# Performance work log

Hardware: AMD Instinct MI355X
Metric: run time of the kernel (lower is better)

Reference implementation:

```python
import jax, jax.numpy as jnp
import numpy as np

B, T, A, S = 8, 64, 4, 512
V, EXT_V = 32000, 33000  # base vocab, base + OOV extensions


def setup_inputs() -> dict:
    key = jax.random.key(0)
    k1, k2, k3, k4, k5 = jax.random.split(key, 5)
    vocab_probs = jax.random.uniform(k1, (B, T, V), dtype=jnp.float32)
    vocab_probs = vocab_probs / vocab_probs.sum(-1, keepdims=True)
    generation_probs = jax.random.uniform(k2, (B, T, A), dtype=jnp.float32)
    agentwise_attn = jax.random.uniform(k3, (B, T, A, S), dtype=jnp.float32)
    agentwise_attn = agentwise_attn / agentwise_attn.sum(-1, keepdims=True)
    agent_attn = jax.random.uniform(k4, (B, T, A), dtype=jnp.float32)
    agent_attn = agent_attn / agent_attn.sum(-1, keepdims=True)
    article = jax.random.randint(k5, (B, A, S), 0, EXT_V, dtype=jnp.int64)
    return {
        "vocab_probs": vocab_probs,
        "generation_probs": generation_probs,
        "agentwise_attn": agentwise_attn,
        "agent_attn": agent_attn,
        "article": article,
    }


def reference(vocab_probs, generation_probs, agentwise_attn, agent_attn, article):
    # vocab_probs: [B,T,V], generation_probs/agent_attn: [B,T,A],
    # agentwise_attn: [B,T,A,S], article: [B,A,S] int indices < EXT_V
    gen = generation_probs[..., None]                       # [B,T,A,1]
    voc_gen = gen * vocab_probs[:, :, None, :]              # [B,T,A,V]
    copy = (1.0 - gen) * agentwise_attn                     # [B,T,A,S]
    # concat-with-zeros pad to extended vocab
    ext = jnp.concatenate(
        [voc_gen, jnp.zeros((B, T, A, EXT_V - V), voc_gen.dtype)], axis=-1
    )                                                       # [B,T,A,EXT_V]
    # scatter_add copy probs at article token positions (expanded over tgt_len)
    idx = jnp.broadcast_to(article[:, None, :, :], (B, T, A, S))
    bi = jnp.arange(B)[:, None, None, None]
    ti = jnp.arange(T)[None, :, None, None]
    ai = jnp.arange(A)[None, None, :, None]
    ext = ext.at[bi, ti, ai, idx].add(copy)
    # agent-attention weighted sum over agents
    return jnp.einsum("bta,btav->btv", agent_attn, ext)     # [B,T,EXT_V]
```

## Files before the change

### kernel.cpp

```cpp
#include <hip/hip_runtime.h>
#include <hip/hip_bf16.h>

constexpr int B = 8, T = 64, A = 4, S = 512;
constexpr int V = 32000, EXT_V = 33000;
constexpr int V4 = V / 4;
constexpr int HALF = EXT_V / 2;
constexpr int H4 = HALF / 4;
constexpr int NTHREADS = 1024;

__global__ void __launch_bounds__(NTHREADS, 2)
fused_kernel(const float* __restrict__ vocab,
             const float* __restrict__ gen,
             const float* __restrict__ attn,
             const float* __restrict__ agent_attn,
             const int* __restrict__ article,
             float* __restrict__ out) {
    __shared__ float smem[HALF];
    const int blk = blockIdx.x;
    const int bt = blk >> 1;
    const int half = blk & 1;
    const int vbase = half * HALF;
    const int b = bt / T;
    const int tid = threadIdx.x;

    float4* s4 = reinterpret_cast<float4*>(smem);
    for (int i = tid; i < H4; i += NTHREADS)
        s4[i] = make_float4(0.f, 0.f, 0.f, 0.f);

    float coef = 0.f;
#pragma unroll
    for (int a = 0; a < A; ++a)
        coef += agent_attn[bt * A + a] * gen[bt * A + a];

    __syncthreads();

#pragma unroll
    for (int k = 0; k < (A * S) / NTHREADS; ++k) {
        const int j = tid + k * NTHREADS;
        const int a = j >> 9;
        const int s = j & (S - 1);
        const int bta = bt * A + a;
        const int idx = article[(b * A + a) * S + s] - vbase;
        if ((unsigned)idx < (unsigned)HALF) {
            const float g = gen[bta];
            const float w = agent_attn[bta] * (1.0f - g);
            const float val = w * attn[(size_t)bta * S + s];
            atomicAdd(smem + idx, val);
        }
    }
    __syncthreads();

    const float4* __restrict__ vrow = reinterpret_cast<const float4*>(vocab + (size_t)bt * V);
    float4* __restrict__ orow = reinterpret_cast<float4*>(out + (size_t)bt * EXT_V);
    const int g4base = vbase / 4;
    for (int i = tid; i < H4; i += NTHREADS) {
        const int gi = g4base + i;
        float4 r = s4[i];
        if (gi < V4) {
            const float4 x = vrow[gi];
            r.x += x.x * coef;
            r.y += x.y * coef;
            r.z += x.z * coef;
            r.w += x.w * coef;
        }
        orow[gi] = r;
    }
}

extern "C" void kernel_launch(void* const* d_in, const int* in_sizes, int n_in,
                              void* d_out, int out_size, void* d_ws, size_t ws_size,
                              hipStream_t stream) {
    const float* vocab      = (const float*)d_in[0];
    const float* gen        = (const float*)d_in[1];
    const float* attn       = (const float*)d_in[2];
    const float* agent_attn = (const float*)d_in[3];
    const int*   article    = (const int*)d_in[4];
    float* out = (float*)d_out;

    fused_kernel<<<2 * B * T, NTHREADS, 0, stream>>>(vocab, gen, attn, agent_attn, article, out);
}
```

Before: 124.6 us.

## Prefetch scatter inputs and first vocab tiles before smem zeroing; remap blocks per XCD

Loads the article indices, attention values and agent weights for the scatter, plus the first two float4 vocab chunks per thread, into registers before the shared-memory clear and first barrier. This hides global-load latency behind the zeroing and the atomics. It also remaps blockIdx so consecutive logical blocks land on the same XCD, which should improve L2 locality for the shared article/gen data. The cost is more live registers under a 1024-thread, 2-blocks-per-CU launch bound.

```diff
diff --git a/kernel.cpp b/kernel.cpp
--- a/kernel.cpp
+++ b/kernel.cpp
@@ -7,6 +7,7 @@
 constexpr int HALF = EXT_V / 2;
 constexpr int H4 = HALF / 4;
 constexpr int NTHREADS = 1024;
+constexpr int NBLK = 2 * B * T;
 
 __global__ void __launch_bounds__(NTHREADS, 2)
 fused_kernel(const float* __restrict__ vocab,
@@ -16,52 +17,65 @@
              const int* __restrict__ article,
              float* __restrict__ out) {
     __shared__ float smem[HALF];
-    const int blk = blockIdx.x;
-    const int bt = blk >> 1;
-    const int half = blk & 1;
+    constexpr int PER_XCD = NBLK / 8;
+    const int l = (blockIdx.x & 7) * PER_XCD + (blockIdx.x >> 3);
+    const int bt = l >> 1;
+    const int half = l & 1;
     const int vbase = half * HALF;
     const int b = bt / T;
     const int tid = threadIdx.x;
 
-    float4* s4 = reinterpret_cast<float4*>(smem);
-    for (int i = tid; i < H4; i += NTHREADS)
-        s4[i] = make_float4(0.f, 0.f, 0.f, 0.f);
+    const int a0 = tid >> 9, s0 = tid & (S - 1);
+    const int j1 = tid + NTHREADS;
+    const int a1 = j1 >> 9, s1 = j1 & (S - 1);
+    const int bta0 = bt * A + a0, bta1 = bt * A + a1;
+    const int idx0 = article[(b * A + a0) * S + s0] - vbase;
+    const int idx1 = article[(b * A + a1) * S + s1] - vbase;
+    const float av0 = attn[(size_t)bta0 * S + s0];
+    const float av1 = attn[(size_t)bta1 * S + s1];
+    const float w0 = agent_attn[bta0] * (1.0f - gen[bta0]);
+    const float w1 = agent_attn[bta1] * (1.0f - gen[bta1]);
 
     float coef = 0.f;
 #pragma unroll
     for (int a = 0; a < A; ++a)
         coef += agent_attn[bt * A + a] * gen[bt * A + a];
 
+    const float4* __restrict__ vrow = reinterpret_cast<const float4*>(vocab + (size_t)bt * V);
+    const int g4base = vbase / 4;
+    const int gi0 = g4base + tid;
+    const int gi1 = g4base + tid + NTHREADS;
+    const bool h0 = gi0 < V4;
+    const bool h1 = gi1 < V4;
+    float4 p0 = h0 ? vrow[gi0] : make_float4(0.f, 0.f, 0.f, 0.f);
+    float4 p1 = h1 ? vrow[gi1] : make_float4(0.f, 0.f, 0.f, 0.f);
+
+    float4* s4 = reinterpret_cast<float4*>(smem);
+    for (int i = tid; i < H4; i += NTHREADS)
+        s4[i] = make_float4(0.f, 0.f, 0.f, 0.f);
     __syncthreads();
 
-#pragma unroll
-    for (int k = 0; k < (A * S) / NTHREADS; ++k) {
-        const int j = tid + k * NTHREADS;
-        const int a = j >> 9;
-        const int s = j & (S - 1);
-        const int bta = bt * A + a;
-        const int idx = article[(b * A + a) * S + s] - vbase;
-        if ((unsigned)idx < (unsigned)HALF) {
-            const float g = gen[bta];
-            const float w = agent_attn[bta] * (1.0f - g);
-            const float val = w * attn[(size_t)bta * S + s];
-            atomicAdd(smem + idx, val);
-        }
-    }
+    if ((unsigned)idx0 < (unsigned)HALF) atomicAdd(smem + idx0, w0 * av0);
+    if ((unsigned)idx1 < (unsigned)HALF) atomicAdd(smem + idx1, w1 * av1);
     __syncthreads();
 
-    const float4* __restrict__ vrow = reinterpret_cast<const float4*>(vocab + (size_t)bt * V);
     float4* __restrict__ orow = reinterpret_cast<float4*>(out + (size_t)bt * EXT_V);
-    const int g4base = vbase / 4;
-    for (int i = tid; i < H4; i += NTHREADS) {
+    {
+        float4 r = s4[tid];
+        r.x += p0.x * coef; r.y += p0.y * coef; r.z += p0.z * coef; r.w += p0.w * coef;
+        orow[gi0] = r;
+    }
+    {
+        float4 r = s4[tid + NTHREADS];
+        r.x += p1.x * coef; r.y += p1.y * coef; r.z += p1.z * coef; r.w += p1.w * coef;
+        orow[gi1] = r;
+    }
+    for (int i = tid + 2 * NTHREADS; i < H4; i += NTHREADS) {
         const int gi = g4base + i;
         float4 r = s4[i];
         if (gi < V4) {
             const float4 x = vrow[gi];
-            r.x += x.x * coef;
-            r.y += x.y * coef;
-            r.z += x.z * coef;
-            r.w += x.w * coef;
+            r.x += x.x * coef; r.y += x.y * coef; r.z += x.z * coef; r.w += x.w * coef;
         }
         orow[gi] = r;
     }
@@ -77,5 +91,5 @@
     const int*   article    = (const int*)d_in[4];
     float* out = (float*)d_out;
 
-    fused_kernel<<<2 * B * T, NTHREADS, 0, stream>>>(vocab, gen, attn, agent_attn, article, out);
+    fused_kernel<<<NBLK, NTHREADS, 0, stream>>>(vocab, gen, attn, agent_attn, article, out);
 }
```

After: 123.0 us. About the same (-1.2%).
